# Optimization experiments

Measured on AMD Instinct MI355X. Metric: run time of the kernel, lower is better.

The kernel has to match this reference:

```python
import jax, jax.numpy as jnp
import numpy as np

TAU = 2.0      # LIF membrane time constant (spikingjelly default-style, decay_input=True)
VTH = 0.5      # v_threshold from init
S = 4          # time_steps
EPS = 1e-5     # BatchNorm eps
ALPHA = 4.0    # surrogate sigmoid alpha (spikingjelly Sigmoid default)

@jax.custom_vjp
def spike(x):
    # Heaviside forward (spikingjelly: x >= 0 -> 1)
    return (x >= 0.0).astype(x.dtype)

def _spike_fwd(x):
    return spike(x), x

def _spike_bwd(x, g):
    sg = jax.nn.sigmoid(ALPHA * x)
    return (g * ALPHA * sg * (1.0 - sg),)

spike.defvjp(_spike_fwd, _spike_bwd)

def bn(y, gamma, beta, mean, var):
    # inference-mode BatchNorm2d over channel axis 1; y: (B, C, T, V)
    inv = gamma * jax.lax.rsqrt(var + EPS)
    return y * inv[None, :, None, None] + (beta - mean * inv)[None, :, None, None]


def setup_inputs() -> dict:
    key = jax.random.key(0)
    ks = jax.random.split(key, 16)
    B, T, C, V, H, NC = 16, 512, 3, 16, 128, 12
    inp = {
        "x": jax.random.normal(ks[0], (B, T, C, V), dtype=jnp.float32),
        "w1": jax.random.normal(ks[1], (H, C), dtype=jnp.float32) * (1.0 / np.sqrt(C)),
        "b1": jax.random.normal(ks[2], (H,), dtype=jnp.float32) * 0.01,
        "g1": jnp.ones((H,), jnp.float32),
        "be1": jnp.zeros((H,), jnp.float32),
        "m1": jax.random.normal(ks[3], (H,), dtype=jnp.float32) * 0.1,
        "rv1": jax.random.uniform(ks[4], (H,), dtype=jnp.float32) + 0.5,
        "w2": jax.random.normal(ks[5], (H, H), dtype=jnp.float32) * (1.0 / np.sqrt(H)),
        "b2": jax.random.normal(ks[6], (H,), dtype=jnp.float32) * 0.01,
        "g2": jnp.ones((H,), jnp.float32),
        "be2": jnp.zeros((H,), jnp.float32),
        "m2": jax.random.normal(ks[7], (H,), dtype=jnp.float32) * 0.1,
        "rv2": jax.random.uniform(ks[8], (H,), dtype=jnp.float32) + 0.5,
        "wc": jax.random.normal(ks[9], (NC, H), dtype=jnp.float32) * (1.0 / np.sqrt(H)),
        "bc": jax.random.normal(ks[10], (NC,), dtype=jnp.float32) * 0.01,
    }
    return inp


def reference(x, w1, b1, g1, be1, m1, rv1, w2, b2, g2, be2, m2, rv2, wc, bc):
    # x: (B, T, C, V) -> channels-first (B, C, T, V) as in torch permute
    xc = jnp.transpose(x, (0, 2, 1, 3))
    # fc1 1x1 conv + BN; input identical across all S steps, so compute once
    h1 = bn(jnp.einsum('bctv,oc->botv', xc, w1) + b1[None, :, None, None],
            g1, be1, m1, rv1)  # (B, H, T, V)

    def step(carry, _):
        v1s, v2s, acc = carry
        # LIF1: decay_input=True, v_reset=0 hard reset
        v1n = v1s + (h1 - v1s) / TAU
        s1 = spike(v1n - VTH)
        v1n = v1n * (1.0 - s1)
        # fc2 1x1 conv + BN on spikes
        h2 = bn(jnp.einsum('botv,po->bptv', s1, w2) + b2[None, :, None, None],
                g2, be2, m2, rv2)
        # LIF2
        v2n = v2s + (h2 - v2s) / TAU
        s2 = spike(v2n - VTH)
        v2n = v2n * (1.0 - s2)
        return (v1n, v2n, acc + s2), None

    z = jnp.zeros_like(h1)
    (_, _, acc), _ = jax.lax.scan(step, (z, z, z), None, length=S)
    # mean over S, then mean over T and V -> (B, H); dropout is identity in eval
    feat = (acc / S).mean(axis=(2, 3))
    return feat @ wc.T + bc
```

## Files before the change

kernel.cpp:

```cpp
#include <hip/hip_runtime.h>
#include <hip/hip_bf16.h>
#include <stdint.h>
#include <math.h>

#define B_ 16
#define T_ 512
#define V_ 16
#define H_ 128
#define NC_ 12

typedef float v2f __attribute__((ext_vector_type(2)));
typedef __attribute__((ext_vector_type(8))) short s8frag;
typedef __attribute__((ext_vector_type(16))) float f16frag;
typedef unsigned long long u64;


__device__ __forceinline__ unsigned short bf16_rne(float w) {
    unsigned u = __float_as_uint(w);
    unsigned r = (u + 0x7FFFu + ((u >> 16) & 1u)) >> 16;
    return (unsigned short)r;
}
__device__ __forceinline__ float bf16_f32(unsigned short h) {
    return __uint_as_float((unsigned)h << 16);
}
__device__ __forceinline__ void split8(const float* __restrict__ s, s8frag& hi, s8frag& lo) {
    #pragma unroll
    for (int j = 0; j < 8; ++j) {
        float w = s[j];
        unsigned short hb = bf16_rne(w);
        unsigned short lb = bf16_rne(w - bf16_f32(hb));
        hi[j] = (short)hb;
        lo[j] = (short)lb;
    }
}
__device__ __forceinline__ uint4 expand8(unsigned bt) {
    uint4 r;
    r.x = ((bt      & 1u) * 0x3F80u) | (((bt >> 1) & 1u) * 0x3F800000u);
    r.y = (((bt >> 2) & 1u) * 0x3F80u) | (((bt >> 3) & 1u) * 0x3F800000u);
    r.z = (((bt >> 4) & 1u) * 0x3F80u) | (((bt >> 5) & 1u) * 0x3F800000u);
    r.w = (((bt >> 6) & 1u) * 0x3F80u) | (((bt >> 7) & 1u) * 0x3F800000u);
    return r;
}

#define ROUNDS 4
__global__ __launch_bounds__(256, 3) void snn_main(
    const float* __restrict__ x,
    const float* __restrict__ w1, const float* __restrict__ b1,
    const float* __restrict__ g1, const float* __restrict__ be1,
    const float* __restrict__ m1, const float* __restrict__ rv1,
    const float* __restrict__ w2, const float* __restrict__ b2,
    const float* __restrict__ g2, const float* __restrict__ be2,
    const float* __restrict__ m2, const float* __restrict__ rv2,
    float* __restrict__ feat)
{
    __shared__ uint4 afrag[2][8][64];
    __shared__ uint4 msk[4][16];
    __shared__ float xs[ROUNDS * 2 * 3 * V_];

    const int tid  = threadIdx.x;
    const int lane = tid & 63;
    const int wv   = tid >> 6;
    const int nl   = lane & 15;
    const int kg   = (lane >> 4) & 1;
    const int ch4  = lane >> 5;
    const int bb   = blockIdx.x >> 7;
    const int sbase = (blockIdx.x & 127) * (ROUNDS * 16);

    if (tid < 48) {
        const float4* xb = (const float4*)(x + ((size_t)(bb * T_ + (sbase >> 4)) * 3) * V_);
        ((float4*)xs)[tid] = xb[tid];
    }

    const int p = lane, q = lane + 64;
    v2f w0v = { w1[p*3+0], w1[q*3+0] };
    v2f w1v = { w1[p*3+1], w1[q*3+1] };
    v2f w2v = { w1[p*3+2], w1[q*3+2] };
    v2f b1v = { b1[p], b1[q] };
    float i1a = g1[p] * (float)(1.0 / sqrt((double)(rv1[p] + 1e-5f)));
    float i1b = g1[q] * (float)(1.0 / sqrt((double)(rv1[q] + 1e-5f)));
    v2f i1v = { i1a, i1b };
    v2f d1v = { be1[p] - m1[p] * i1a, be1[q] - m1[q] * i1b };

    const int chn = wv * 32 + (lane & 31);
    float i2c = g2[chn] * (float)(1.0 / sqrt((double)(rv2[chn] + 1e-5f)));
    float d2c = be2[chn] - m2[chn] * i2c;
    float dd2 = fmaf(b2[chn], i2c, d2c);

    s8frag bh[8], bl[8];
    #pragma unroll
    for (int c = 0; c < 8; ++c)
        split8(&w2[chn * H_ + c * 16 + ch4 * 8], bh[c], bl[c]);

    __syncthreads();

    float facc = 0.f;
    f16frag acc0, acc1;

    for (int r = 0; r < ROUNDS; ++r) {
        #pragma unroll
        for (int i = 0; i < 4; ++i) {
            int ls = r * 16 + wv * 4 + i;
            int tl = ls >> 4, v = ls & 15;
            const float* xp = &xs[tl * 48 + v];
            float x0 = xp[0], x1 = xp[V_], x2 = xp[2 * V_];

            v2f h1 = ((x0 * w0v + x1 * w1v + x2 * w2v) + b1v) * i1v + d1v;
            v2f v1t = h1 * 0.5f;
            v2f v2t = v1t + h1 * 0.25f;
            v2f v3t = v2t + (h1 - v2t) * 0.5f;
            v2f v4t = v3t + (h1 - v3t) * 0.5f;

            u64 t1a = __ballot(v1t.x >= 0.5f), t2a = __ballot(v2t.x >= 0.5f);
            u64 t3a = __ballot(v3t.x >= 0.5f), t4a = __ballot(v4t.x >= 0.5f);
            u64 t1b = __ballot(v1t.y >= 0.5f), t2b = __ballot(v2t.y >= 0.5f);
            u64 t3b = __ballot(v3t.y >= 0.5f), t4b = __ballot(v4t.y >= 0.5f);
            u64 s3a = t1a | (t3a & ~t2a), s3b = t1b | (t3b & ~t2b);
            u64 s4a = t2a | (t4a & ~t3a), s4b = t2b | (t4b & ~t3b);

            u64 mx = (lane == 0) ? t1a : (lane == 1) ? t2a : (lane == 2) ? s3a : s4a;
            u64 my = (lane == 0) ? t1b : (lane == 1) ? t2b : (lane == 2) ? s3b : s4b;
            if (lane < 4) {
                uint4 mm;
                mm.x = (unsigned)mx; mm.y = (unsigned)(mx >> 32);
                mm.z = (unsigned)my; mm.w = (unsigned)(my >> 32);
                msk[wv][i * 4 + lane] = mm;
            }
        }
        {
            uint4 mm = msk[wv][nl];
            u64 wsel = ch4 ? ((u64)mm.z | ((u64)mm.w << 32))
                           : ((u64)mm.x | ((u64)mm.y << 32));
            int tt   = wv >> 1;
            int slot = ((wv & 1) * 16 + nl) + 32 * kg;
            #pragma unroll
            for (int j = 0; j < 4; ++j) {
                unsigned by = (unsigned)(wsel >> (kg * 8 + j * 16)) & 0xFFu;
                afrag[tt][ch4 * 4 + j][slot] = expand8(by);
            }
        }
        __syncthreads();

        acc0 = (f16frag){0.f,0.f,0.f,0.f,0.f,0.f,0.f,0.f,
                         0.f,0.f,0.f,0.f,0.f,0.f,0.f,0.f};
        acc1 = acc0;
        __builtin_amdgcn_s_setprio(1);
        #pragma unroll
        for (int c = 0; c < 8; ++c) {
            s8frag a0 = *(const s8frag*)&afrag[0][c][lane];
            s8frag a1 = *(const s8frag*)&afrag[1][c][lane];
            acc0 = __builtin_amdgcn_mfma_f32_32x32x16_bf16(a0, bh[c], acc0, 0,0,0);
            acc1 = __builtin_amdgcn_mfma_f32_32x32x16_bf16(a1, bh[c], acc1, 0,0,0);
            acc0 = __builtin_amdgcn_mfma_f32_32x32x16_bf16(a0, bl[c], acc0, 0,0,0);
            acc1 = __builtin_amdgcn_mfma_f32_32x32x16_bf16(a1, bl[c], acc1, 0,0,0);
        }
        __builtin_amdgcn_s_setprio(0);
        if (r + 1 < ROUNDS) __syncthreads();

        #pragma unroll
        for (int tt = 0; tt < 2; ++tt) {
            const f16frag accs = tt ? acc1 : acc0;
            #pragma unroll
            for (int g = 0; g < 4; ++g) {
                float v = 0.f;
                #pragma unroll
                for (int s = 0; s < 4; ++s) {
                    float h2 = fmaf(accs[g*4+s], i2c, dd2);
                    v = v + (h2 - v) * 0.5f;
                    bool sp = v >= 0.5f;
                    v = sp ? 0.f : v;
                    facc += sp ? 1.f : 0.f;
                }
            }
        }
    }

    facc += __shfl_xor(facc, 32);
    if (lane < 32) atomicAdd(&feat[bb * H_ + chn], facc);
}

__global__ __launch_bounds__(128) void classifier_kernel(
    const float* __restrict__ feat,
    const float* __restrict__ wc,
    const float* __restrict__ bc,
    float* __restrict__ out) {
    __shared__ float fb[H_];
    int b = blockIdx.x, t = threadIdx.x;
    fb[t] = feat[b * H_ + t] * (1.0f / 32768.0f);
    __syncthreads();
    if (t < NC_) {
        float s = 0.f;
        for (int h = 0; h < H_; ++h) s += fb[h] * wc[t * H_ + h];
        out[b * NC_ + t] = s + bc[t];
    }
}

extern "C" void kernel_launch(void* const* d_in, const int* in_sizes, int n_in,
                              void* d_out, int out_size, void* d_ws, size_t ws_size,
                              hipStream_t stream) {
    const float* x   = (const float*)d_in[0];
    const float* w1  = (const float*)d_in[1];
    const float* b1  = (const float*)d_in[2];
    const float* g1  = (const float*)d_in[3];
    const float* be1 = (const float*)d_in[4];
    const float* m1  = (const float*)d_in[5];
    const float* rv1 = (const float*)d_in[6];
    const float* w2  = (const float*)d_in[7];
    const float* b2  = (const float*)d_in[8];
    const float* g2  = (const float*)d_in[9];
    const float* be2 = (const float*)d_in[10];
    const float* m2  = (const float*)d_in[11];
    const float* rv2 = (const float*)d_in[12];
    const float* wc  = (const float*)d_in[13];
    const float* bc  = (const float*)d_in[14];

    float* feat = (float*)d_ws;
    float* out  = (float*)d_out;

    snn_main<<<2048, 256, 0, stream>>>(x, w1, b1, g1, be1, m1, rv1,
                                       w2, b2, g2, be2, m2, rv2, feat);
    classifier_kernel<<<B_, 128, 0, stream>>>(feat, wc, bc, out);
}
```

Baseline: 138.7 us.

## Batch two rounds per barrier pair by enlarging shared A-fragment buffer

Restructures the main loop so each super-round builds spike masks for 32 spatial slots (8 per wave) into a doubled afrag buffer, then runs two MFMA passes before the next barrier. This halves the number of __syncthreads per block while keeping the same total work. It costs more LDS (afrag doubles) and longer per-wave mask-building phases, which may reduce occupancy or overlap between waves.

```diff
diff --git a/kernel.cpp b/kernel.cpp
--- a/kernel.cpp
+++ b/kernel.cpp
@@ -42,7 +42,7 @@
     return r;
 }
 
-#define ROUNDS 4
+#define SROUNDS 2
 __global__ __launch_bounds__(256, 3) void snn_main(
     const float* __restrict__ x,
     const float* __restrict__ w1, const float* __restrict__ b1,
@@ -53,18 +53,17 @@
     const float* __restrict__ m2, const float* __restrict__ rv2,
     float* __restrict__ feat)
 {
-    __shared__ uint4 afrag[2][8][64];
-    __shared__ uint4 msk[4][16];
-    __shared__ float xs[ROUNDS * 2 * 3 * V_];
+    __shared__ uint4 afrag[4][8][64];
+    __shared__ uint4 msk[4][32];
+    __shared__ float xs[4 * 3 * V_];
 
     const int tid  = threadIdx.x;
     const int lane = tid & 63;
     const int wv   = tid >> 6;
-    const int nl   = lane & 15;
-    const int kg   = (lane >> 4) & 1;
-    const int ch4  = lane >> 5;
+    const int row  = lane & 31;
+    const int half = lane >> 5;
     const int bb   = blockIdx.x >> 7;
-    const int sbase = (blockIdx.x & 127) * (ROUNDS * 16);
+    const int sbase = (blockIdx.x & 127) * (SROUNDS * 32);
 
     if (tid < 48) {
         const float4* xb = (const float4*)(x + ((size_t)(bb * T_ + (sbase >> 4)) * 3) * V_);
@@ -89,17 +88,16 @@
     s8frag bh[8], bl[8];
     #pragma unroll
     for (int c = 0; c < 8; ++c)
-        split8(&w2[chn * H_ + c * 16 + ch4 * 8], bh[c], bl[c]);
+        split8(&w2[chn * H_ + c * 16 + half * 8], bh[c], bl[c]);
 
     __syncthreads();
 
     float facc = 0.f;
-    f16frag acc0, acc1;
-
-    for (int r = 0; r < ROUNDS; ++r) {
+
+    for (int sr = 0; sr < SROUNDS; ++sr) {
         #pragma unroll
-        for (int i = 0; i < 4; ++i) {
-            int ls = r * 16 + wv * 4 + i;
+        for (int i = 0; i < 8; ++i) {
+            int ls = sr * 32 + wv * 8 + i;
             int tl = ls >> 4, v = ls & 15;
             const float* xp = &xs[tl * 48 + v];
             float x0 = xp[0], x1 = xp[V_], x2 = xp[2 * V_];
@@ -127,51 +125,54 @@
             }
         }
         {
-            uint4 mm = msk[wv][nl];
-            u64 wsel = ch4 ? ((u64)mm.z | ((u64)mm.w << 32))
-                           : ((u64)mm.x | ((u64)mm.y << 32));
-            int tt   = wv >> 1;
-            int slot = ((wv & 1) * 16 + nl) + 32 * kg;
+            uint4 mm = msk[wv][row];
+            u64 wsel = half ? ((u64)mm.z | ((u64)mm.w << 32))
+                            : ((u64)mm.x | ((u64)mm.y << 32));
             #pragma unroll
-            for (int j = 0; j < 4; ++j) {
-                unsigned by = (unsigned)(wsel >> (kg * 8 + j * 16)) & 0xFFu;
-                afrag[tt][ch4 * 4 + j][slot] = expand8(by);
-            }
+            for (int kg = 0; kg < 2; ++kg)
+                #pragma unroll
+                for (int j = 0; j < 4; ++j) {
+                    unsigned by = (unsigned)(wsel >> (kg * 8 + j * 16)) & 0xFFu;
+                    afrag[wv][half * 4 + j][row + 32 * kg] = expand8(by);
+                }
         }
         __syncthreads();
 
-        acc0 = (f16frag){0.f,0.f,0.f,0.f,0.f,0.f,0.f,0.f,
-                         0.f,0.f,0.f,0.f,0.f,0.f,0.f,0.f};
-        acc1 = acc0;
-        __builtin_amdgcn_s_setprio(1);
         #pragma unroll
-        for (int c = 0; c < 8; ++c) {
-            s8frag a0 = *(const s8frag*)&afrag[0][c][lane];
-            s8frag a1 = *(const s8frag*)&afrag[1][c][lane];
-            acc0 = __builtin_amdgcn_mfma_f32_32x32x16_bf16(a0, bh[c], acc0, 0,0,0);
-            acc1 = __builtin_amdgcn_mfma_f32_32x32x16_bf16(a1, bh[c], acc1, 0,0,0);
-            acc0 = __builtin_amdgcn_mfma_f32_32x32x16_bf16(a0, bl[c], acc0, 0,0,0);
-            acc1 = __builtin_amdgcn_mfma_f32_32x32x16_bf16(a1, bl[c], acc1, 0,0,0);
-        }
-        __builtin_amdgcn_s_setprio(0);
-        if (r + 1 < ROUNDS) __syncthreads();
-
-        #pragma unroll
-        for (int tt = 0; tt < 2; ++tt) {
-            const f16frag accs = tt ? acc1 : acc0;
+        for (int tp = 0; tp < 2; ++tp) {
+            f16frag acc0 = {0.f,0.f,0.f,0.f,0.f,0.f,0.f,0.f,
+                            0.f,0.f,0.f,0.f,0.f,0.f,0.f,0.f};
+            f16frag acc1 = acc0;
+            __builtin_amdgcn_s_setprio(1);
             #pragma unroll
-            for (int g = 0; g < 4; ++g) {
-                float v = 0.f;
+            for (int c = 0; c < 8; ++c) {
+                s8frag a0 = *(const s8frag*)&afrag[tp * 2][c][lane];
+                s8frag a1 = *(const s8frag*)&afrag[tp * 2 + 1][c][lane];
+                acc0 = __builtin_amdgcn_mfma_f32_32x32x16_bf16(a0, bh[c], acc0, 0,0,0);
+                acc1 = __builtin_amdgcn_mfma_f32_32x32x16_bf16(a1, bh[c], acc1, 0,0,0);
+                acc0 = __builtin_amdgcn_mfma_f32_32x32x16_bf16(a0, bl[c], acc0, 0,0,0);
+                acc1 = __builtin_amdgcn_mfma_f32_32x32x16_bf16(a1, bl[c], acc1, 0,0,0);
+            }
+            __builtin_amdgcn_s_setprio(0);
+
+            #pragma unroll
+            for (int tt = 0; tt < 2; ++tt) {
+                const f16frag accs = tt ? acc1 : acc0;
                 #pragma unroll
-                for (int s = 0; s < 4; ++s) {
-                    float h2 = fmaf(accs[g*4+s], i2c, dd2);
-                    v = v + (h2 - v) * 0.5f;
-                    bool sp = v >= 0.5f;
-                    v = sp ? 0.f : v;
-                    facc += sp ? 1.f : 0.f;
+                for (int g = 0; g < 4; ++g) {
+                    float v = 0.f;
+                    #pragma unroll
+                    for (int s = 0; s < 4; ++s) {
+                        float h2 = fmaf(accs[g*4+s], i2c, dd2);
+                        v = v + (h2 - v) * 0.5f;
+                        bool sp = v >= 0.5f;
+                        v = sp ? 0.f : v;
+                        facc += sp ? 1.f : 0.f;
+                    }
                 }
             }
         }
+        if (sr + 1 < SROUNDS) __syncthreads();
     }
 
     facc += __shfl_xor(facc, 32);
```

Result: slower. 141.6 us (+2.1%).
